# Performance work log

Hardware: AMD Instinct MI355X
Metric: run time of the kernel (lower is better)

## Reference

```python
import jax, jax.numpy as jnp
import numpy as np

L, C, H = 12, 1024, 16  # n_layer, n_embd, n_head
D = C // H
EPS = 1e-5

def gelu_new(x):
    # GPT-2 tanh-approximate GELU
    return 0.5 * x * (1.0 + jnp.tanh(np.sqrt(2.0 / np.pi).astype(np.float32) * (x + 0.044715 * x ** 3)))

def layernorm(x, g, b):
    mu = jnp.mean(x, axis=-1, keepdims=True)
    var = jnp.mean(jnp.square(x - mu), axis=-1, keepdims=True)
    return (x - mu) * jax.lax.rsqrt(var + EPS) * g + b

def setup_inputs() -> dict:
    key = jax.random.key(0)
    ks = jax.random.split(key, 8)
    std = 0.02
    inp = {
        'inputs_embeds': jax.random.normal(ks[0], (1, 1024, C), jnp.float32),
        'attention_mask': jnp.ones((1, 1024), jnp.float32),
        'ln1_g': jnp.ones((L, C), jnp.float32), 'ln1_b': jnp.zeros((L, C), jnp.float32),
        'Wqkv': jax.random.normal(ks[1], (L, C, 3 * C), jnp.float32) * std,
        'bqkv': jnp.zeros((L, 3 * C), jnp.float32),
        'Wo': jax.random.normal(ks[2], (L, C, C), jnp.float32) * (std / np.sqrt(2 * L)),
        'bo': jnp.zeros((L, C), jnp.float32),
        'ln2_g': jnp.ones((L, C), jnp.float32), 'ln2_b': jnp.zeros((L, C), jnp.float32),
        'Wfc': jax.random.normal(ks[3], (L, C, 4 * C), jnp.float32) * std,
        'bfc': jnp.zeros((L, 4 * C), jnp.float32),
        'Wmp': jax.random.normal(ks[4], (L, 4 * C, C), jnp.float32) * (std / np.sqrt(2 * L)),
        'bmp': jnp.zeros((L, C), jnp.float32),
        'lnf_g': jnp.ones((C,), jnp.float32), 'lnf_b': jnp.zeros((C,), jnp.float32),
    }
    return inp

def reference(inputs_embeds, attention_mask, ln1_g, ln1_b, Wqkv, bqkv, Wo, bo,
              ln2_g, ln2_b, Wfc, bfc, Wmp, bmp, lnf_g, lnf_b):
    B, T, _ = inputs_embeds.shape
    # padding mask -> additive bias [B,1,1,T] (broadcasts over heads and query dim)
    mask_add = -1e9 * (1.0 - attention_mask)[:, None, None, :]
    scale = 1.0 / np.sqrt(D).astype(np.float32)

    def block(x, p):
        g1, b1, Wq, bq, Wo_, bo_, g2, b2, Wf, bf, Wm, bm = p
        h = layernorm(x, g1, b1)
        qkv = h @ Wq + bq                                  # [B,T,3C]
        q, k, v = jnp.split(qkv, 3, axis=-1)
        q = q.reshape(B, T, H, D).transpose(0, 2, 1, 3)    # [B,H,T,D]
        k = k.reshape(B, T, H, D).transpose(0, 2, 1, 3)
        v = v.reshape(B, T, H, D).transpose(0, 2, 1, 3)
        att = jnp.einsum('bhqd,bhkd->bhqk', q, k) * scale + mask_add
        att = jax.nn.softmax(att, axis=-1)
        y = jnp.einsum('bhqk,bhkd->bhqd', att, v)
        y = y.transpose(0, 2, 1, 3).reshape(B, T, C)
        x = x + (y @ Wo_ + bo_)
        h2 = layernorm(x, g2, b2)
        x = x + (gelu_new(h2 @ Wf + bf) @ Wm + bm)
        return x, None

    params = (ln1_g, ln1_b, Wqkv, bqkv, Wo, bo, ln2_g, ln2_b, Wfc, bfc, Wmp, bmp)
    x, _ = jax.lax.scan(block, inputs_embeds, params)
    return layernorm(x, lnf_g, lnf_b)
```

## Files before the change

kernel.cpp:

```cpp
#include <hip/hip_runtime.h>
#include <hip/hip_bf16.h>
#include <math.h>

#define LN_EPS 1e-5f

typedef unsigned short u16;
typedef __attribute__((ext_vector_type(8))) _Float16 f16x8;
typedef __attribute__((ext_vector_type(4))) float f32x4;

__device__ __forceinline__ u16 f2h(float x) {
    _Float16 h = (_Float16)x;
    return __builtin_bit_cast(u16, h);
}
__device__ __forceinline__ void stv(float* p, float v) { *p = v; }
__device__ __forceinline__ void stv(u16* p, float v) { *p = f2h(v); }
__device__ __forceinline__ void stv4(float* p, float a, float b, float c, float d) {
    *(float4*)p = make_float4(a, b, c, d);
}
__device__ __forceinline__ void stv4(u16* p, float a, float b, float c, float d) {
    ushort4 o; o.x = f2h(a); o.y = f2h(b); o.z = f2h(c); o.w = f2h(d);
    *(ushort4*)p = o;
}

__device__ __forceinline__ float gelu_f(float x) {
    const float kA = 0.7978845608028654f;
    return 0.5f * x * (1.f + tanhf(kA * (x + 0.044715f * x * x * x)));
}

__device__ __forceinline__ void gl_lds16(const u16* g, u16* l) {
    __builtin_amdgcn_global_load_lds(
        (const __attribute__((address_space(1))) unsigned int*)g,
        (__attribute__((address_space(3))) unsigned int*)l, 16, 0, 0);
}
template <int N> __device__ __forceinline__ void s_vmcnt() {
    asm volatile("s_waitcnt vmcnt(%0)" :: "n"(N) : "memory");
}
__device__ __forceinline__ void s_lgkm0() {
    asm volatile("s_waitcnt lgkmcnt(0)" ::: "memory");
    __builtin_amdgcn_sched_barrier(0);
}
__device__ __forceinline__ void bar() { __builtin_amdgcn_s_barrier(); }
__device__ __forceinline__ void sfence() { __builtin_amdgcn_sched_barrier(0); }

template <typename OT>
__global__ __launch_bounds__(256) void ln_kernel(const float* __restrict__ x,
                                                 const float* __restrict__ gam,
                                                 const float* __restrict__ bet,
                                                 OT* __restrict__ out) {
    int w = threadIdx.x >> 6, lane = threadIdx.x & 63;
    int row = blockIdx.x * 4 + w;
    const float* xr = x + (size_t)row * 1024;
    float4 v[4];
    float s = 0.f, ss = 0.f;
#pragma unroll
    for (int j = 0; j < 4; j++) {
        v[j] = *(const float4*)(xr + lane * 4 + j * 256);
        s += v[j].x + v[j].y + v[j].z + v[j].w;
        ss += v[j].x * v[j].x + v[j].y * v[j].y + v[j].z * v[j].z + v[j].w * v[j].w;
    }
#pragma unroll
    for (int off = 32; off > 0; off >>= 1) {
        s += __shfl_xor(s, off);
        ss += __shfl_xor(ss, off);
    }
    float mu = s * (1.f / 1024.f);
    float var = ss * (1.f / 1024.f) - mu * mu;
    float rstd = rsqrtf(var + LN_EPS);
#pragma unroll
    for (int j = 0; j < 4; j++) {
        int c = lane * 4 + j * 256;
        float4 gv = *(const float4*)(gam + c);
        float4 bv = *(const float4*)(bet + c);
        stv4(&out[(size_t)row * 1024 + c],
             (v[j].x - mu) * rstd * gv.x + bv.x,
             (v[j].y - mu) * rstd * gv.y + bv.y,
             (v[j].z - mu) * rstd * gv.z + bv.z,
             (v[j].w - mu) * rstd * gv.w + bv.w);
    }
}

__global__ __launch_bounds__(256) void tr_cvt_all(
    const float* __restrict__ Wqkv, const float* __restrict__ Wo,
    const float* __restrict__ Wfc, const float* __restrict__ Wmp,
    u16* __restrict__ wq, u16* __restrict__ wo,
    u16* __restrict__ wf, u16* __restrict__ wm) {
    int id = blockIdx.x;
    const float* W; u16* Wt; int K, N, idx;
    if (id < 768)       { W = Wqkv; Wt = wq; K = 1024; N = 3072; idx = id; }
    else if (id < 1024) { W = Wo;   Wt = wo; K = 1024; N = 1024; idx = id - 768; }
    else if (id < 2048) { W = Wfc;  Wt = wf; K = 1024; N = 4096; idx = id - 1024; }
    else                { W = Wmp;  Wt = wm; K = 4096; N = 1024; idx = id - 2048; }
    int ntn = N >> 6;
    int n0 = (idx % ntn) * 64, k0 = (idx / ntn) * 64;

    __shared__ float tile[64][65];
    int t = threadIdx.x;
    int r = t >> 4, c4 = (t & 15) * 4;
#pragma unroll
    for (int p = 0; p < 4; p++) {
        float4 v = *(const float4*)(W + (size_t)(k0 + p * 16 + r) * N + n0 + c4);
        tile[p * 16 + r][c4 + 0] = v.x;
        tile[p * 16 + r][c4 + 1] = v.y;
        tile[p * 16 + r][c4 + 2] = v.z;
        tile[p * 16 + r][c4 + 3] = v.w;
    }
    __syncthreads();
#pragma unroll
    for (int p = 0; p < 4; p++) {
        int n = p * 16 + r;
        ushort4 o;
        o.x = f2h(tile[c4 + 0][n]);
        o.y = f2h(tile[c4 + 1][n]);
        o.z = f2h(tile[c4 + 2][n]);
        o.w = f2h(tile[c4 + 3][n]);
        *(ushort4*)(Wt + (size_t)(n0 + n) * K + k0 + c4) = o;
    }
}

template <int BM, int BN, int BK, int ACT, int RES, int WVT, typename OT>
__global__ __launch_bounds__(256) void gemm_f16(
    const u16* __restrict__ A, const u16* __restrict__ Bt,
    const float* __restrict__ bias, const float* __restrict__ res,
    OT* __restrict__ out, u16* __restrict__ vTout, int M, int N, int K) {
    __shared__ u16 As[2][BM * BK];
    __shared__ u16 Bs[2][BN * BK];
    constexpr int WM = BM / 2, WN = BN / 2;
    constexpr int FM = WM / 16, FN = WN / 16;
    constexpr int NKF = BK / 32;
    constexpr int SLOTS = BK / 8;
    constexpr int ACH = BM * BK / 8 / 256;
    constexpr int BCH = BN * BK / 8 / 256;
    constexpr int LPS = ACH + BCH;
    int tid = threadIdx.x;
    int w = tid >> 6, l = tid & 63;
    int wm = w >> 1, wn = w & 1;
    int lr = l & 15, g = l >> 4;
    int m0 = blockIdx.y * BM, n0 = blockIdx.x * BN;

    f32x4 acc[FM][FN] = {};

    auto stage = [&](int buf, int k0) {
#pragma unroll
        for (int i = 0; i < ACH; i++) {
            int chunk = i * 256 + tid;
            int row = chunk / SLOTS, s = chunk % SLOTS, sg = s ^ (row & 7);
            gl_lds16(A + (size_t)(m0 + row) * K + k0 + sg * 8, &As[buf][chunk * 8]);
        }
#pragma unroll
        for (int i = 0; i < BCH; i++) {
            int chunk = i * 256 + tid;
            int row = chunk / SLOTS, s = chunk % SLOTS, sg = s ^ (row & 7);
            gl_lds16(Bt + (size_t)(n0 + row) * K + k0 + sg * 8, &Bs[buf][chunk * 8]);
        }
    };

    int NT = K / BK;
    stage(0, 0);
    int cur = 0;
    for (int t = 0; t < NT; t++) {
        if (t + 1 < NT) { stage(cur ^ 1, (t + 1) * BK); s_vmcnt<LPS>(); }
        else            { s_vmcnt<0>(); }
        bar();
        sfence();

        const u16* Ab = &As[cur][0];
        const u16* Bb = &Bs[cur][0];
        f16x8 af[FM][NKF], bfrag[FN][NKF];
#pragma unroll
        for (int m = 0; m < FM; m++)
#pragma unroll
            for (int kf = 0; kf < NKF; kf++) {
                int row = wm * WM + m * 16 + lr;
                af[m][kf] = *(const f16x8*)(Ab + row * BK + (((kf * 4 + g) ^ (row & 7)) * 8));
            }
#pragma unroll
        for (int n = 0; n < FN; n++)
#pragma unroll
            for (int kf = 0; kf < NKF; kf++) {
                int row = wn * WN + n * 16 + lr;
                bfrag[n][kf] = *(const f16x8*)(Bb + row * BK + (((kf * 4 + g) ^ (row & 7)) * 8));
            }
#pragma unroll
        for (int kf = 0; kf < NKF; kf++)
#pragma unroll
            for (int m = 0; m < FM; m++)
#pragma unroll
                for (int n = 0; n < FN; n++)
                    acc[m][n] = __builtin_amdgcn_mfma_f32_16x16x32_f16(
                        af[m][kf], bfrag[n][kf], acc[m][n], 0, 0, 0);

        sfence();
        bar();
        cur ^= 1;
    }

#pragma unroll
    for (int m = 0; m < FM; m++) {
#pragma unroll
        for (int n = 0; n < FN; n++) {
            int col = n0 + wn * WN + n * 16 + lr;
            int row0 = m0 + wm * WM + m * 16 + 4 * g;
            float bv = bias[col];
            u16 hv[4];
#pragma unroll
            for (int r = 0; r < 4; r++) {
                float v = acc[m][n][r] + bv;
                if (ACT) v = gelu_f(v);
                if (RES) v += res[(size_t)(row0 + r) * N + col];
                stv(&out[(size_t)(row0 + r) * N + col], v);
                hv[r] = f2h(v);
            }
            if (WVT && col >= 2048) {
                ushort4 pv; pv.x = hv[0]; pv.y = hv[1]; pv.z = hv[2]; pv.w = hv[3];
                *(ushort4*)(vTout + (size_t)(col - 2048) * 1024 + row0) = pv;
            }
        }
    }
}

__global__ __launch_bounds__(256) void attn_mfma(
    const u16* __restrict__ qkv, const u16* __restrict__ vT,
    const float* __restrict__ mask, u16* __restrict__ y) {
    int h = blockIdx.y;
    int q0 = blockIdx.x * 64;
    int tid = threadIdx.x;
    int w = tid >> 6, l = tid & 63;
    int lr = l & 15, g = l >> 4;

    __shared__ u16 Ks[2][128 * 64];
    __shared__ u16 Vs[2][64 * 128];
    __shared__ u16 Ps[4 * 16 * 128];
    __shared__ float maskb[1024];

    for (int i = tid; i < 1024; i += 256) maskb[i] = -1e9f * (1.f - mask[i]);
    s_lgkm0();

    f16x8 qf[2];
#pragma unroll
    for (int kf = 0; kf < 2; kf++)
        qf[kf] = *(const f16x8*)(qkv + (size_t)(q0 + w * 16 + lr) * 3072 + h * 64 + kf * 32 + g * 8);

    f32x4 o[4] = {};
    float mrow[4], lrow[4];
#pragma unroll
    for (int r = 0; r < 4; r++) { mrow[r] = -1e30f; lrow[r] = 0.f; }

    u16* Psw = Ps + w * 2048;

    auto stage = [&](int buf, int kc) {
#pragma unroll
        for (int i = 0; i < 4; i++) {
            int chunk = i * 256 + tid;
            int krow = chunk >> 3, ks = chunk & 7, ksg = ks ^ (krow & 7);
            gl_lds16(qkv + (size_t)(kc * 128 + krow) * 3072 + 1024 + h * 64 + ksg * 8,
                     &Ks[buf][chunk * 8]);
            int vrow = chunk >> 4, vs = chunk & 15, vsg = vs ^ (vrow & 7);
            gl_lds16(vT + (size_t)(h * 64 + vrow) * 1024 + kc * 128 + vsg * 8,
                     &Vs[buf][chunk * 8]);
        }
    };

    stage(0, 0);
    int cur = 0;
    for (int kc = 0; kc < 8; kc++) {
        if (kc + 1 < 8) { stage(cur ^ 1, kc + 1); s_vmcnt<8>(); }
        else            { s_vmcnt<0>(); }
        bar();
        sfence();
        const u16* Kb = &Ks[cur][0];
        const u16* Vb = &Vs[cur][0];

        f32x4 s[8] = {};
        __builtin_amdgcn_s_setprio(1);
#pragma unroll
        for (int n = 0; n < 8; n++)
#pragma unroll
            for (int kf = 0; kf < 2; kf++) {
                int row = n * 16 + lr;
                f16x8 kfrag = *(const f16x8*)(Kb + row * 64 + (((kf * 4 + g) ^ (row & 7)) * 8));
                s[n] = __builtin_amdgcn_mfma_f32_16x16x32_f16(qf[kf], kfrag, s[n], 0, 0, 0);
            }
        __builtin_amdgcn_s_setprio(0);

        float mcol[8];
#pragma unroll
        for (int n = 0; n < 8; n++) mcol[n] = maskb[kc * 128 + n * 16 + lr];

        float scl[4], mnew[4], psum[4];
#pragma unroll
        for (int r = 0; r < 4; r++) {
            float mx = -1e30f;
#pragma unroll
            for (int n = 0; n < 8; n++) {
                float sv = s[n][r] * 0.125f + mcol[n];
                s[n][r] = sv;
                mx = fmaxf(mx, sv);
            }
            mx = fmaxf(mx, __shfl_xor(mx, 1));
            mx = fmaxf(mx, __shfl_xor(mx, 2));
            mx = fmaxf(mx, __shfl_xor(mx, 4));
            mx = fmaxf(mx, __shfl_xor(mx, 8));
            mnew[r] = fmaxf(mrow[r], mx);
            scl[r] = __expf(mrow[r] - mnew[r]);
            mrow[r] = mnew[r];
            psum[r] = 0.f;
        }
#pragma unroll
        for (int n = 0; n < 8; n++) {
            float p0 = __expf(s[n][0] - mnew[0]);
            float p1 = __expf(s[n][1] - mnew[1]);
            float p2 = __expf(s[n][2] - mnew[2]);
            float p3 = __expf(s[n][3] - mnew[3]);
            psum[0] += p0; psum[1] += p1; psum[2] += p2; psum[3] += p3;
            int col = n * 16 + lr, cs = col >> 3, cl = col & 7;
            int r0 = 4 * g;
            Psw[(r0 + 0) * 128 + ((cs ^ ((r0 + 0) & 7)) * 8) + cl] = f2h(p0);
            Psw[(r0 + 1) * 128 + ((cs ^ ((r0 + 1) & 7)) * 8) + cl] = f2h(p1);
            Psw[(r0 + 2) * 128 + ((cs ^ ((r0 + 2) & 7)) * 8) + cl] = f2h(p2);
            Psw[(r0 + 3) * 128 + ((cs ^ ((r0 + 3) & 7)) * 8) + cl] = f2h(p3);
        }
#pragma unroll
        for (int r = 0; r < 4; r++) {
            float ps_ = psum[r];
            ps_ += __shfl_xor(ps_, 1);
            ps_ += __shfl_xor(ps_, 2);
            ps_ += __shfl_xor(ps_, 4);
            ps_ += __shfl_xor(ps_, 8);
            lrow[r] = lrow[r] * scl[r] + ps_;
#pragma unroll
            for (int dn = 0; dn < 4; dn++) o[dn][r] *= scl[r];
        }

        f16x8 pa[4];
#pragma unroll
        for (int kf = 0; kf < 4; kf++)
            pa[kf] = *(const f16x8*)(Psw + lr * 128 + (((kf * 4 + g) ^ (lr & 7)) * 8));
        __builtin_amdgcn_s_setprio(1);
#pragma unroll
        for (int dn = 0; dn < 4; dn++) {
#pragma unroll
            for (int kf = 0; kf < 4; kf++) {
                int row = dn * 16 + lr;
                f16x8 vb = *(const f16x8*)(Vb + row * 128 + (((kf * 4 + g) ^ (row & 7)) * 8));
                o[dn] = __builtin_amdgcn_mfma_f32_16x16x32_f16(pa[kf], vb, o[dn], 0, 0, 0);
            }
        }
        __builtin_amdgcn_s_setprio(0);

        sfence();
        bar();
        cur ^= 1;
    }

    float inv[4];
#pragma unroll
    for (int r = 0; r < 4; r++) inv[r] = 1.f / lrow[r];
#pragma unroll
    for (int dn = 0; dn < 4; dn++)
#pragma unroll
        for (int r = 0; r < 4; r++) {
            int row = q0 + w * 16 + 4 * g + r;
            int col = h * 64 + dn * 16 + lr;
            y[(size_t)row * 1024 + col] = f2h(o[dn][r] * inv[r]);
        }
}

extern "C" void kernel_launch(void* const* d_in, const int* in_sizes, int n_in,
                              void* d_out, int out_size, void* d_ws, size_t ws_size,
                              hipStream_t stream) {
    const float* inputs_embeds = (const float*)d_in[0];
    const float* attn_mask     = (const float*)d_in[1];
    const float* ln1_g = (const float*)d_in[2];
    const float* ln1_b = (const float*)d_in[3];
    const float* Wqkv  = (const float*)d_in[4];
    const float* bqkv  = (const float*)d_in[5];
    const float* Wo    = (const float*)d_in[6];
    const float* bo    = (const float*)d_in[7];
    const float* ln2_g = (const float*)d_in[8];
    const float* ln2_b = (const float*)d_in[9];
    const float* Wfc   = (const float*)d_in[10];
    const float* bfc   = (const float*)d_in[11];
    const float* Wmp   = (const float*)d_in[12];
    const float* bmp   = (const float*)d_in[13];
    const float* lnf_g = (const float*)d_in[14];
    const float* lnf_b = (const float*)d_in[15];
    float* out = (float*)d_out;

    char* ws = (char*)d_ws;
    float* x   = (float*)ws;
    u16* hbuf  = (u16*)(ws + (4u << 20));
    u16* qkvb  = (u16*)(ws + (6u << 20));
    u16* fcb   = qkvb;
    u16* ybuf  = hbuf;
    u16* vTb   = (u16*)(ws + (14u << 20));
    u16* wq    = (u16*)(ws + (16u << 20));
    u16* wo_   = (u16*)(ws + (22u << 20));
    u16* wf    = (u16*)(ws + (24u << 20));
    u16* wm    = (u16*)(ws + (32u << 20));

    hipMemcpyAsync(x, inputs_embeds, (size_t)(1 << 20) * sizeof(float),
                   hipMemcpyDeviceToDevice, stream);

    for (int l = 0; l < 12; l++) {
        tr_cvt_all<<<3072, 256, 0, stream>>>(
            Wqkv + (size_t)l * 3145728, Wo + (size_t)l * 1048576,
            Wfc + (size_t)l * 4194304, Wmp + (size_t)l * 4194304,
            wq, wo_, wf, wm);

        ln_kernel<u16><<<256, 256, 0, stream>>>(x, ln1_g + l * 1024, ln1_b + l * 1024, hbuf);
        gemm_f16<64, 128, 64, 0, 0, 1, u16><<<dim3(24, 16), 256, 0, stream>>>(
            hbuf, wq, bqkv + (size_t)l * 3072, nullptr, qkvb, vTb, 1024, 3072, 1024);
        attn_mfma<<<dim3(16, 16), 256, 0, stream>>>(qkvb, vTb, attn_mask, ybuf);
        gemm_f16<64, 64, 128, 0, 1, 0, float><<<dim3(16, 16), 256, 0, stream>>>(
            ybuf, wo_, bo + (size_t)l * 1024, x, x, nullptr, 1024, 1024, 1024);
        ln_kernel<u16><<<256, 256, 0, stream>>>(x, ln2_g + l * 1024, ln2_b + l * 1024, hbuf);
        gemm_f16<128, 128, 64, 1, 0, 0, u16><<<dim3(32, 8), 256, 0, stream>>>(
            hbuf, wf, bfc + (size_t)l * 4096, nullptr, fcb, nullptr, 1024, 4096, 1024);
        gemm_f16<64, 64, 128, 0, 1, 0, float><<<dim3(16, 16), 256, 0, stream>>>(
            fcb, wm, bmp + (size_t)l * 1024, x, x, nullptr, 1024, 1024, 4096);
    }
    ln_kernel<float><<<256, 256, 0, stream>>>(x, lnf_g, lnf_b, out);
}
```

Before: 1.576 ms.

## Split-K the projection GEMMs and fold the residual add into LayerNorm

```diff
diff --git a/kernel.cpp b/kernel.cpp
--- a/kernel.cpp
+++ b/kernel.cpp
@@ -42,21 +42,32 @@
 __device__ __forceinline__ void bar() { __builtin_amdgcn_s_barrier(); }
 __device__ __forceinline__ void sfence() { __builtin_amdgcn_sched_barrier(0); }
 
-template <typename OT>
-__global__ __launch_bounds__(256) void ln_kernel(const float* __restrict__ x,
+template <int PART, typename OT>
+__global__ __launch_bounds__(256) void ln_kernel(float* __restrict__ x,
+                                                 const float* __restrict__ p0,
+                                                 const float* __restrict__ p1,
                                                  const float* __restrict__ gam,
                                                  const float* __restrict__ bet,
                                                  OT* __restrict__ out) {
     int w = threadIdx.x >> 6, lane = threadIdx.x & 63;
     int row = blockIdx.x * 4 + w;
-    const float* xr = x + (size_t)row * 1024;
+    size_t base = (size_t)row * 1024;
     float4 v[4];
     float s = 0.f, ss = 0.f;
 #pragma unroll
     for (int j = 0; j < 4; j++) {
-        v[j] = *(const float4*)(xr + lane * 4 + j * 256);
-        s += v[j].x + v[j].y + v[j].z + v[j].w;
-        ss += v[j].x * v[j].x + v[j].y * v[j].y + v[j].z * v[j].z + v[j].w * v[j].w;
+        int c = lane * 4 + j * 256;
+        float4 xv = *(const float4*)(x + base + c);
+        if (PART) {
+            float4 a = *(const float4*)(p0 + base + c);
+            float4 b = *(const float4*)(p1 + base + c);
+            xv.x += a.x + b.x; xv.y += a.y + b.y;
+            xv.z += a.z + b.z; xv.w += a.w + b.w;
+            *(float4*)(x + base + c) = xv;
+        }
+        v[j] = xv;
+        s += xv.x + xv.y + xv.z + xv.w;
+        ss += xv.x * xv.x + xv.y * xv.y + xv.z * xv.z + xv.w * xv.w;
     }
 #pragma unroll
     for (int off = 32; off > 0; off >>= 1) {
@@ -71,7 +82,7 @@
         int c = lane * 4 + j * 256;
         float4 gv = *(const float4*)(gam + c);
         float4 bv = *(const float4*)(bet + c);
-        stv4(&out[(size_t)row * 1024 + c],
+        stv4(&out[base + c],
              (v[j].x - mu) * rstd * gv.x + bv.x,
              (v[j].y - mu) * rstd * gv.y + bv.y,
              (v[j].z - mu) * rstd * gv.z + bv.z,
@@ -117,44 +128,49 @@
     }
 }
 
-template <int BM, int BN, int BK, int ACT, int RES, int WVT, typename OT>
-__global__ __launch_bounds__(256) void gemm_f16(
+template <int BM, int BN, int BK, int WROW, int WCOL, int ACT, int WVT, int SPLITK,
+          typename OT>
+__global__ __launch_bounds__(WROW * WCOL * 64) void gemm_f16(
     const u16* __restrict__ A, const u16* __restrict__ Bt,
-    const float* __restrict__ bias, const float* __restrict__ res,
-    OT* __restrict__ out, u16* __restrict__ vTout, int M, int N, int K) {
+    const float* __restrict__ bias, OT* __restrict__ out,
+    u16* __restrict__ vTout, int M, int N, int K) {
     __shared__ u16 As[2][BM * BK];
     __shared__ u16 Bs[2][BN * BK];
-    constexpr int WM = BM / 2, WN = BN / 2;
+    constexpr int THREADS = WROW * WCOL * 64;
+    constexpr int WM = BM / WROW, WN = BN / WCOL;
     constexpr int FM = WM / 16, FN = WN / 16;
     constexpr int NKF = BK / 32;
     constexpr int SLOTS = BK / 8;
-    constexpr int ACH = BM * BK / 8 / 256;
-    constexpr int BCH = BN * BK / 8 / 256;
+    constexpr int ACH = BM * BK / 8 / THREADS;
+    constexpr int BCH = BN * BK / 8 / THREADS;
     constexpr int LPS = ACH + BCH;
     int tid = threadIdx.x;
     int w = tid >> 6, l = tid & 63;
-    int wm = w >> 1, wn = w & 1;
+    int wm = w / WCOL, wn = w % WCOL;
     int lr = l & 15, g = l >> 4;
     int m0 = blockIdx.y * BM, n0 = blockIdx.x * BN;
+    int kbase = (SPLITK > 1) ? blockIdx.z * (K / SPLITK) : 0;
+    int Kc = (SPLITK > 1) ? (K / SPLITK) : K;
+    OT* outz = (SPLITK > 1) ? out + (size_t)blockIdx.z * M * N : out;
 
     f32x4 acc[FM][FN] = {};
 
     auto stage = [&](int buf, int k0) {
 #pragma unroll
         for (int i = 0; i < ACH; i++) {
-            int chunk = i * 256 + tid;
+            int chunk = i * THREADS + tid;
             int row = chunk / SLOTS, s = chunk % SLOTS, sg = s ^ (row & 7);
-            gl_lds16(A + (size_t)(m0 + row) * K + k0 + sg * 8, &As[buf][chunk * 8]);
+            gl_lds16(A + (size_t)(m0 + row) * K + kbase + k0 + sg * 8, &As[buf][chunk * 8]);
         }
 #pragma unroll
         for (int i = 0; i < BCH; i++) {
-            int chunk = i * 256 + tid;
+            int chunk = i * THREADS + tid;
             int row = chunk / SLOTS, s = chunk % SLOTS, sg = s ^ (row & 7);
-            gl_lds16(Bt + (size_t)(n0 + row) * K + k0 + sg * 8, &Bs[buf][chunk * 8]);
+            gl_lds16(Bt + (size_t)(n0 + row) * K + kbase + k0 + sg * 8, &Bs[buf][chunk * 8]);
         }
     };
 
-    int NT = K / BK;
+    int NT = Kc / BK;
     stage(0, 0);
     int cur = 0;
     for (int t = 0; t < NT; t++) {
@@ -200,15 +216,14 @@
         for (int n = 0; n < FN; n++) {
             int col = n0 + wn * WN + n * 16 + lr;
             int row0 = m0 + wm * WM + m * 16 + 4 * g;
-            float bv = bias[col];
+            float bv = (SPLITK > 1 && blockIdx.z != 0) ? 0.f : bias[col];
             u16 hv[4];
 #pragma unroll
             for (int r = 0; r < 4; r++) {
                 float v = acc[m][n][r] + bv;
                 if (ACT) v = gelu_f(v);
-                if (RES) v += res[(size_t)(row0 + r) * N + col];
-                stv(&out[(size_t)(row0 + r) * N + col], v);
-                hv[r] = f2h(v);
+                stv(&outz[(size_t)(row0 + r) * N + col], v);
+                if (WVT) hv[r] = f2h(v);
             }
             if (WVT && col >= 2048) {
                 ushort4 pv; pv.x = hv[0]; pv.y = hv[1]; pv.z = hv[2]; pv.w = hv[3];
@@ -397,6 +412,8 @@
     u16* wo_   = (u16*)(ws + (22u << 20));
     u16* wf    = (u16*)(ws + (24u << 20));
     u16* wm    = (u16*)(ws + (32u << 20));
+    float* pP  = (float*)(ws + (40u << 20));
+    float* pM  = (float*)(ws + (48u << 20));
 
     hipMemcpyAsync(x, inputs_embeds, (size_t)(1 << 20) * sizeof(float),
                    hipMemcpyDeviceToDevice, stream);
@@ -407,17 +424,24 @@
             Wfc + (size_t)l * 4194304, Wmp + (size_t)l * 4194304,
             wq, wo_, wf, wm);
 
-        ln_kernel<u16><<<256, 256, 0, stream>>>(x, ln1_g + l * 1024, ln1_b + l * 1024, hbuf);
-        gemm_f16<64, 128, 64, 0, 0, 1, u16><<<dim3(24, 16), 256, 0, stream>>>(
-            hbuf, wq, bqkv + (size_t)l * 3072, nullptr, qkvb, vTb, 1024, 3072, 1024);
+        if (l == 0)
+            ln_kernel<0, u16><<<256, 256, 0, stream>>>(
+                x, nullptr, nullptr, ln1_g + l * 1024, ln1_b + l * 1024, hbuf);
+        else
+            ln_kernel<1, u16><<<256, 256, 0, stream>>>(
+                x, pM, pM + (1 << 20), ln1_g + l * 1024, ln1_b + l * 1024, hbuf);
+
+        gemm_f16<64, 128, 64, 2, 2, 0, 1, 1, u16><<<dim3(24, 16), 256, 0, stream>>>(
+            hbuf, wq, bqkv + (size_t)l * 3072, qkvb, vTb, 1024, 3072, 1024);
         attn_mfma<<<dim3(16, 16), 256, 0, stream>>>(qkvb, vTb, attn_mask, ybuf);
-        gemm_f16<64, 64, 128, 0, 1, 0, float><<<dim3(16, 16), 256, 0, stream>>>(
-            ybuf, wo_, bo + (size_t)l * 1024, x, x, nullptr, 1024, 1024, 1024);
-        ln_kernel<u16><<<256, 256, 0, stream>>>(x, ln2_g + l * 1024, ln2_b + l * 1024, hbuf);
-        gemm_f16<128, 128, 64, 1, 0, 0, u16><<<dim3(32, 8), 256, 0, stream>>>(
-            hbuf, wf, bfc + (size_t)l * 4096, nullptr, fcb, nullptr, 1024, 4096, 1024);
-        gemm_f16<64, 64, 128, 0, 1, 0, float><<<dim3(16, 16), 256, 0, stream>>>(
-            fcb, wm, bmp + (size_t)l * 1024, x, x, nullptr, 1024, 1024, 4096);
-    }
-    ln_kernel<float><<<256, 256, 0, stream>>>(x, lnf_g, lnf_b, out);
-}
+        gemm_f16<64, 64, 128, 2, 2, 0, 0, 2, float><<<dim3(16, 16, 2), 256, 0, stream>>>(
+            ybuf, wo_, bo + (size_t)l * 1024, pP, nullptr, 1024, 1024, 1024);
+        ln_kernel<1, u16><<<256, 256, 0, stream>>>(
+            x, pP, pP + (1 << 20), ln2_g + l * 1024, ln2_b + l * 1024, hbuf);
+        gemm_f16<128, 128, 64, 2, 4, 1, 0, 1, u16><<<dim3(32, 8), 512, 0, stream>>>(
+            hbuf, wf, bfc + (size_t)l * 4096, fcb, nullptr, 1024, 4096, 1024);
+        gemm_f16<64, 64, 128, 2, 2, 0, 0, 2, float><<<dim3(16, 16, 2), 256, 0, stream>>>(
+            fcb, wm, bmp + (size_t)l * 1024, pM, nullptr, 1024, 1024, 4096);
+    }
+    ln_kernel<1, float><<<256, 256, 0, stream>>>(x, pM, pM + (1 << 20), lnf_g, lnf_b, out);
+}
```

After: 1.373 ms. -12.9%, faster.
